# Kernel tuning notes

Hardware: AMD Instinct MI355X
Metric: run time of the kernel (lower is better)

Reference implementation:

```python
import jax, jax.numpy as jnp
import numpy as np

R = 32            # voxel resolution
DIM = 240         # channels C
EPS_NORM = 0.0    # module eps
BN_EPS = 1e-5     # torch BatchNorm1d default eps


def setup_inputs() -> dict:
    key = jax.random.key(0)
    k1, k2, k3 = jax.random.split(key, 3)
    B, C, N = 4, DIM, 32768
    features = jax.random.normal(k1, (B, C, N), jnp.float32)
    coords = jax.random.uniform(k2, (B, 3, N), jnp.float32)
    # mlp params: Conv1d(2C -> C, kernel 1) + BatchNorm1d(C)
    w = jax.random.normal(k3, (C, 2 * C), jnp.float32) / np.sqrt(2 * C).astype(np.float32)
    b = jnp.zeros((C,), jnp.float32)
    gamma = jnp.ones((C,), jnp.float32)
    beta = jnp.zeros((C,), jnp.float32)
    return {"features": features, "coords": coords, "w": w, "b": b, "gamma": gamma, "beta": beta}


def _voxelize(features, coords):
    # normalize coords into [0, 1], scale to voxel grid
    nc = coords - coords.mean(axis=2, keepdims=True)                      # [B,3,N]
    scale = jnp.linalg.norm(nc, axis=1, keepdims=True).max(axis=2, keepdims=True) * 2.0 + EPS_NORM
    nc = nc / scale + 0.5
    nc = jnp.clip(nc * R, 0, R - 1)
    vox = jnp.round(nc).astype(jnp.int32)
    pos = vox[:, 0] + vox[:, 1] * R + vox[:, 2] * (R * R)                 # [B,N] flattened voxel id
    R3 = R * R * R

    def per_batch(f, p):
        # f: [C,N], p: [N] -> [2C, R3]; per-voxel max feature + second (min) feature
        mx = jax.ops.segment_max(f.T, p, num_segments=R3)                 # [R3, C]
        mn = jax.ops.segment_min(f.T, p, num_segments=R3)                 # [R3, C]
        cnt = jax.ops.segment_sum(jnp.ones_like(p), p, num_segments=R3)  # [R3]
        mask = (cnt > 0)[:, None]
        mx = jnp.where(mask, mx, 0.0)
        mn = jnp.where(mask, mn, 0.0)
        return jnp.concatenate([mx, mn], axis=1).T                        # [2C, R3]

    fea = jax.vmap(per_batch)(features, pos)                              # [B,2C,R3]
    return fea, nc


def reference(features, coords, w, b, gamma, beta):
    fea, nc = _voxelize(features, coords)
    # 1x1 Conv1d (pointwise GEMM) + BatchNorm1d (training-mode batch stats) + Swish
    y = jnp.einsum('co,bov->bcv', w, fea) + b[None, :, None]
    mean = y.mean(axis=(0, 2), keepdims=True)
    var = y.var(axis=(0, 2), keepdims=True)
    y = gamma[None, :, None] * (y - mean) * jax.lax.rsqrt(var + BN_EPS) + beta[None, :, None]
    y = y * jax.nn.sigmoid(y)
    B, C, _ = features.shape
    return y.reshape(B, C, R, R, R), nc
```

## Files before the change

kernel.cpp:

```cpp
#include <hip/hip_runtime.h>
#include <cstdint>
#include <cstddef>

#define RR 32
#define R3 32768
#define NPT 32768
#define CH 240
#define CH2 480
#define NB 4
#define Y_ELEMS 31457280

typedef __attribute__((ext_vector_type(8))) short short8v;
typedef __attribute__((ext_vector_type(4))) float float4v;

union u8pack { short8v v; unsigned short u[8]; };

static __device__ __forceinline__ float bf2f(unsigned short u) {
  return __uint_as_float(((unsigned int)u) << 16);
}
static __device__ __forceinline__ unsigned short f2bf(float f) {
  unsigned int u = __float_as_uint(f);
  u = (u + 0x7FFFu + ((u >> 16) & 1u)) >> 16;
  return (unsigned short)u;
}

__global__ void k_init(int* __restrict__ cnt, float* __restrict__ stats,
                       const float* __restrict__ w, unsigned short* __restrict__ wfrag) {
  int g = blockIdx.x * 256 + threadIdx.x;
  if (g < NB * R3) cnt[g] = 0;
  if (g < 4096) stats[g] = 0.0f;
  if (g < 14400) {
    int lane = g & 63, t = g >> 6;
    int mg = t / 75, r = t % 75;
    int kc = r / 5, mL = r % 5;
    int m = mg * 5 + mL;
    int ln = lane & 15, q = lane >> 4;
    const float* src = w + (size_t)(m * 16 + ln) * CH2 + kc * 32 + q * 8;
    u8pack pk;
#pragma unroll
    for (int j = 0; j < 8; j++) pk.u[j] = f2bf(src[j]);
    *(short8v*)&wfrag[(size_t)g * 8] = pk.v;
  }
}

__global__ __launch_bounds__(1024) void k_coord_stats(const float* __restrict__ coords,
                                                      float* __restrict__ ms) {
  __shared__ float red[1024];
  __shared__ float mean[3];
  int b = blockIdx.x, t = threadIdx.x;
  const float4* cb4 = (const float4*)(coords + (size_t)b * 3 * NPT);
  float s[3] = {0.f, 0.f, 0.f};
  for (int i = t; i < NPT / 4; i += 1024) {
#pragma unroll
    for (int d = 0; d < 3; d++) {
      float4 v = cb4[d * (NPT / 4) + i];
      s[d] += (v.x + v.y) + (v.z + v.w);
    }
  }
  for (int d = 0; d < 3; d++) {
    red[t] = s[d]; __syncthreads();
    for (int k = 512; k > 0; k >>= 1) { if (t < k) red[t] += red[t + k]; __syncthreads(); }
    if (t == 0) mean[d] = red[0] * (1.0f / NPT);
    __syncthreads();
  }
  float m0 = mean[0], m1 = mean[1], m2 = mean[2];
  float mx = 0.f;
  for (int i = t; i < NPT / 4; i += 1024) {
    float4 x = cb4[i], y = cb4[NPT / 4 + i], z = cb4[2 * (NPT / 4) + i];
    float dx, dy, dz, n;
    dx = x.x - m0; dy = y.x - m1; dz = z.x - m2; n = dx * dx + dy * dy + dz * dz; mx = fmaxf(mx, n);
    dx = x.y - m0; dy = y.y - m1; dz = z.y - m2; n = dx * dx + dy * dy + dz * dz; mx = fmaxf(mx, n);
    dx = x.z - m0; dy = y.z - m1; dz = z.z - m2; n = dx * dx + dy * dy + dz * dz; mx = fmaxf(mx, n);
    dx = x.w - m0; dy = y.w - m1; dz = z.w - m2; n = dx * dx + dy * dy + dz * dz; mx = fmaxf(mx, n);
  }
  red[t] = mx; __syncthreads();
  for (int k = 512; k > 0; k >>= 1) { if (t < k) red[t] = fmaxf(red[t], red[t + k]); __syncthreads(); }
  if (t == 0) {
    ms[b * 4 + 0] = m0; ms[b * 4 + 1] = m1; ms[b * 4 + 2] = m2;
    ms[b * 4 + 3] = sqrtf(red[0]) * 2.0f;
  }
}

__global__ void k_pos_nc(const float* __restrict__ coords, const float* __restrict__ ms,
                         float* __restrict__ ncout, int* __restrict__ pos, int* __restrict__ cnt) {
  int g = blockIdx.x * 256 + threadIdx.x;
  int b = g >> 15, i = g & (NPT - 1);
  const float* cb = coords + (size_t)b * 3 * NPT;
  float scale = ms[b * 4 + 3];
  int vox[3];
#pragma unroll
  for (int d = 0; d < 3; d++) {
    float v = (cb[(size_t)d * NPT + i] - ms[b * 4 + d]) / scale + 0.5f;
    v = fminf(fmaxf(v * (float)RR, 0.0f), (float)(RR - 1));
    ncout[((size_t)(b * 3 + d)) * NPT + i] = v;
    vox[d] = (int)rintf(v);
  }
  int p = (b << 15) | (vox[0] + (vox[1] << 5) + (vox[2] << 10));
  pos[g] = p;
  atomicAdd(&cnt[p], 1);
}

__global__ void k_scan(const int* __restrict__ cnt, int* __restrict__ offs) {
  __shared__ int part[1024];
  int b = blockIdx.x, t = threadIdx.x;
  const int base = b * R3;
  int local[32];
  int s = 0;
#pragma unroll
  for (int j = 0; j < 32; j++) { local[j] = cnt[base + t * 32 + j]; s += local[j]; }
  part[t] = s; __syncthreads();
  for (int d = 1; d < 1024; d <<= 1) {
    int v = (t >= d) ? part[t - d] : 0;
    __syncthreads();
    part[t] += v;
    __syncthreads();
  }
  int run = (t == 0) ? 0 : part[t - 1];
#pragma unroll
  for (int j = 0; j < 32; j++) { offs[base + t * 32 + j] = run; run += local[j]; }
}

__global__ void k_scatter(const int* __restrict__ pos, int* __restrict__ offs,
                          int* __restrict__ rank) {
  int g = blockIdx.x * 256 + threadIdx.x;
  int p = pos[g];
  int slot = atomicAdd(&offs[p], 1);
  rank[g] = slot;
}

__global__ void k_transpose3(const float* __restrict__ f, const int* __restrict__ rank,
                             unsigned short* __restrict__ fts) {
  __shared__ float tile[CH * 65];
  __shared__ int slts[64];
  int p0 = blockIdx.x * 64, b = blockIdx.y;
  int t = threadIdx.x;
  if (t < 64) slts[t] = rank[b * NPT + p0 + t];
  {
    int pp = t & 63, cq = t >> 6;
    const float* src = f + ((size_t)b * CH) * NPT + p0 + pp;
#pragma unroll 4
    for (int j = 0; j < 60; ++j) {
      int c = j * 4 + cq;
      tile[c * 65 + pp] = src[(size_t)c * NPT];
    }
  }
  __syncthreads();
  int ch8 = t & 7;
#pragma unroll
  for (int pass = 0; pass < 2; ++pass) {
    int p = pass * 32 + (t >> 3);
    unsigned short* dst = fts + ((size_t)(b * NPT + slts[p])) * CH;
#pragma unroll
    for (int i = 0; i < 4; ++i) {
      int ch = ch8 + 8 * i;
      if (ch < 30) {
        u8pack pk;
#pragma unroll
        for (int jj = 0; jj < 8; ++jj) pk.u[jj] = f2bf(tile[(ch * 8 + jj) * 65 + p]);
        *(short8v*)&dst[ch * 8] = pk.v;
      }
    }
  }
}

__global__ __launch_bounds__(512, 4) void k_fused(const int* __restrict__ cnt,
                                                  const int* __restrict__ offs,
                                                  const unsigned short* __restrict__ fts,
                                                  const unsigned short* __restrict__ wfrag,
                                                  const float* __restrict__ bias,
                                                  unsigned short* __restrict__ ybf,
                                                  float* __restrict__ gstats) {
  __shared__ unsigned short fB[4 * 15 * 512];
  __shared__ float bstats[480];
  __shared__ int scnt[64];
  __shared__ int soffs[64];
  int tid = threadIdx.x;
  int wave = tid >> 6, lane = tid & 63;
  int sub = lane >> 5, l = lane & 31;
  int ln = lane & 15, q = lane >> 4;
  int b = blockIdx.y;
  int v0 = blockIdx.x * 64;
  int bbase = b << 15;

  for (int i = tid; i < 480; i += 512) bstats[i] = 0.0f;
  if (tid < 64) scnt[tid] = cnt[bbase + v0 + tid];
  else if (tid < 128) soffs[tid - 64] = offs[bbase + v0 + (tid - 64)];
  __syncthreads();

  int proc = wave * 2 + sub;
  int t1c = 30 + l;
  int kc0 = l >> 2, q0 = l & 3;
  int kc1 = t1c >> 2, q1 = t1c & 3;
#pragma unroll 1
  for (int it = 0; it < 4; ++it) {
    if (l < 30) {
      int lv = it * 16 + proc;
      int ci0 = (q0 * 16 + proc) ^ (kc0 & 7);
      int ci1 = (q1 * 16 + proc) ^ (kc1 & 7);
      int idx0 = ((it * 15 + kc0) * 64 + ci0) * 8;
      int idx1 = ((it * 15 + kc1) * 64 + ci1) * 8;
      int n = scnt[lv];
      if (n == 0) {
        u8pack z;
#pragma unroll
        for (int k = 0; k < 8; k++) z.u[k] = 0;
        *(short8v*)&fB[idx0] = z.v;
        *(short8v*)&fB[idx1] = z.v;
      } else {
        int start = soffs[lv] - n;
        const unsigned short* sp = fts + (size_t)(bbase + start) * CH + l * 8;
        float mx[8], mn[8];
#pragma unroll
        for (int k = 0; k < 8; k++) { mx[k] = -__builtin_inff(); mn[k] = __builtin_inff(); }
        int j = 0;
        for (; j + 8 <= n; j += 8) {
          u8pack u0, u1, u2, u3, u4, u5, u6, u7;
          u0.v = *(const short8v*)(sp);
          u1.v = *(const short8v*)(sp + CH);
          u2.v = *(const short8v*)(sp + 2 * CH);
          u3.v = *(const short8v*)(sp + 3 * CH);
          u4.v = *(const short8v*)(sp + 4 * CH);
          u5.v = *(const short8v*)(sp + 5 * CH);
          u6.v = *(const short8v*)(sp + 6 * CH);
          u7.v = *(const short8v*)(sp + 7 * CH);
          sp += 8 * CH;
#pragma unroll
          for (int k = 0; k < 8; k++) {
            float a0 = bf2f(u0.u[k]), a1 = bf2f(u1.u[k]);
            float a2 = bf2f(u2.u[k]), a3 = bf2f(u3.u[k]);
            float a4 = bf2f(u4.u[k]), a5 = bf2f(u5.u[k]);
            float a6 = bf2f(u6.u[k]), a7 = bf2f(u7.u[k]);
            float hx = fmaxf(fmaxf(fmaxf(a0, a1), fmaxf(a2, a3)),
                             fmaxf(fmaxf(a4, a5), fmaxf(a6, a7)));
            float hn = fminf(fminf(fminf(a0, a1), fminf(a2, a3)),
                             fminf(fminf(a4, a5), fminf(a6, a7)));
            mx[k] = fmaxf(mx[k], hx);
            mn[k] = fminf(mn[k], hn);
          }
        }
        for (; j + 2 <= n; j += 2) {
          u8pack u0, u1;
          u0.v = *(const short8v*)(sp);
          u1.v = *(const short8v*)(sp + CH);
          sp += 2 * CH;
#pragma unroll
          for (int k = 0; k < 8; k++) {
            float a0 = bf2f(u0.u[k]), a1 = bf2f(u1.u[k]);
            mx[k] = fmaxf(mx[k], fmaxf(a0, a1));
            mn[k] = fminf(mn[k], fminf(a0, a1));
          }
        }
        if (j < n) {
          u8pack u0;
          u0.v = *(const short8v*)(sp);
#pragma unroll
          for (int k = 0; k < 8; k++) {
            float a = bf2f(u0.u[k]);
            mx[k] = fmaxf(mx[k], a);
            mn[k] = fminf(mn[k], a);
          }
        }
        u8pack omx, omn;
#pragma unroll
        for (int k = 0; k < 8; k++) { omx.u[k] = f2bf(mx[k]); omn.u[k] = f2bf(mn[k]); }
        *(short8v*)&fB[idx0] = omx.v;
        *(short8v*)&fB[idx1] = omn.v;
      }
    }
  }

  int nmt = (wave == 7) ? 1 : 2;
  short8v wreg[2][15];
#pragma unroll
  for (int mm = 0; mm < 2; ++mm)
    if (mm < nmt) {
      int mt = wave * 2 + mm;
      int mg = mt / 5, mL = mt % 5;
      const unsigned short* wp = wfrag + ((size_t)(mg * 75 + mL) * 512) + lane * 8;
#pragma unroll
      for (int kc = 0; kc < 15; ++kc)
        wreg[mm][kc] = *(const short8v*)(wp + (size_t)kc * 5 * 512);
    }

  __syncthreads();

  float4v acc[2][4];
#pragma unroll
  for (int mm = 0; mm < 2; ++mm)
#pragma unroll
    for (int cg = 0; cg < 4; ++cg) acc[mm][cg] = (float4v){0.f, 0.f, 0.f, 0.f};

#pragma unroll
  for (int kc = 0; kc < 15; ++kc) {
    const unsigned short* fbl = fB + (size_t)((lane ^ (kc & 7)) * 8);
    short8v bf[4];
#pragma unroll
    for (int cg = 0; cg < 4; ++cg)
      bf[cg] = *(const short8v*)(fbl + (size_t)(cg * 15 + kc) * 512);
#pragma unroll
    for (int mm = 0; mm < 2; ++mm)
      if (mm < nmt)
#pragma unroll
        for (int cg = 0; cg < 4; ++cg)
          acc[mm][cg] = __builtin_amdgcn_mfma_f32_16x16x32_bf16(wreg[mm][kc], bf[cg], acc[mm][cg], 0, 0, 0);
  }

  unsigned short* yb = ybf + ((size_t)b * CH) * R3 + v0 + ln;
#pragma unroll
  for (int mm = 0; mm < 2; ++mm)
    if (mm < nmt) {
      int mt = wave * 2 + mm;
#pragma unroll
      for (int r = 0; r < 4; ++r) {
        int c = mt * 16 + q * 4 + r;
        float bb = bias[c];
        unsigned short* yrow = yb + (size_t)c * R3;
        float s = 0.f, sq = 0.f;
#pragma unroll
        for (int cg = 0; cg < 4; ++cg) {
          float yv = acc[mm][cg][r] + bb;
          yrow[cg * 16] = f2bf(yv);
          s += yv; sq += yv * yv;
        }
#pragma unroll
        for (int off = 1; off < 16; off <<= 1) {
          s += __shfl_xor(s, off);
          sq += __shfl_xor(sq, off);
        }
        if (ln == 0) {
          atomicAdd(&bstats[c], s);
          atomicAdd(&bstats[240 + c], sq);
        }
      }
    }
  __syncthreads();
  float* gslot = gstats + (size_t)(blockIdx.x & 7) * 512;
  for (int i = tid; i < 480; i += 512) {
    int g = (i < 240) ? i : (256 + (i - 240));
    atomicAdd(&gslot[g], bstats[(i < 240) ? i : (240 + (i - 240))]);
  }
}

__global__ void k_apply(const unsigned short* __restrict__ ybf, float* __restrict__ out,
                        const float* __restrict__ stats, const float* __restrict__ gamma,
                        const float* __restrict__ beta) {
  int g = blockIdx.x * 256 + threadIdx.x;
  int c = (g >> 12) % CH;
  const float ninv = 1.0f / (float)(NB * R3);
  float sum = 0.f, ssq = 0.f;
#pragma unroll
  for (int sl = 0; sl < 8; ++sl) {
    sum += stats[sl * 512 + c];
    ssq += stats[sl * 512 + 256 + c];
  }
  float mean = sum * ninv;
  float var = ssq * ninv - mean * mean;
  float s = gamma[c] * rsqrtf(var + 1e-5f);
  float h = beta[c] - mean * s;
  u8pack v;
  v.v = *(const short8v*)(ybf + (size_t)g * 8);
  float4 o0, o1;
  float t;
  t = bf2f(v.u[0]) * s + h; o0.x = t / (1.0f + __expf(-t));
  t = bf2f(v.u[1]) * s + h; o0.y = t / (1.0f + __expf(-t));
  t = bf2f(v.u[2]) * s + h; o0.z = t / (1.0f + __expf(-t));
  t = bf2f(v.u[3]) * s + h; o0.w = t / (1.0f + __expf(-t));
  t = bf2f(v.u[4]) * s + h; o1.x = t / (1.0f + __expf(-t));
  t = bf2f(v.u[5]) * s + h; o1.y = t / (1.0f + __expf(-t));
  t = bf2f(v.u[6]) * s + h; o1.z = t / (1.0f + __expf(-t));
  t = bf2f(v.u[7]) * s + h; o1.w = t / (1.0f + __expf(-t));
  ((float4*)out)[(size_t)g * 2] = o0;
  ((float4*)out)[(size_t)g * 2 + 1] = o1;
}

extern "C" void kernel_launch(void* const* d_in, const int* in_sizes, int n_in,
                              void* d_out, int out_size, void* d_ws, size_t ws_size,
                              hipStream_t stream) {
  const float* features = (const float*)d_in[0];
  const float* coords   = (const float*)d_in[1];
  const float* w        = (const float*)d_in[2];
  const float* bias     = (const float*)d_in[3];
  const float* gamma    = (const float*)d_in[4];
  const float* beta     = (const float*)d_in[5];
  float* out = (float*)d_out;

  char* ws = (char*)d_ws;
  size_t off = 0;
  float* ms    = (float*)(ws + off); off += 256;
  float* stats = (float*)(ws + off); off += 16384;
  int* pos     = (int*)(ws + off);   off += (size_t)NB * NPT * 4;
  int* cnt     = (int*)(ws + off);   off += (size_t)NB * R3 * 4;
  int* offs    = (int*)(ws + off);   off += (size_t)NB * R3 * 4;
  int* rank    = (int*)(ws + off);   off += (size_t)NB * NPT * 4;
  unsigned short* wfrag = (unsigned short*)(ws + off); off += (size_t)CH * CH2 * 2;
  unsigned short* fts   = (unsigned short*)(ws + off); off += (size_t)NB * NPT * CH * 2;
  unsigned short* ybf   = (unsigned short*)(ws + off); off += (size_t)NB * R3 * CH * 2;

  float* ncout = out + Y_ELEMS;

  k_init<<<516, 256, 0, stream>>>(cnt, stats, w, wfrag);
  k_coord_stats<<<4, 1024, 0, stream>>>(coords, ms);
  k_pos_nc<<<512, 256, 0, stream>>>(coords, ms, ncout, pos, cnt);
  k_scan<<<4, 1024, 0, stream>>>(cnt, offs);
  k_scatter<<<512, 256, 0, stream>>>(pos, offs, rank);
  k_transpose3<<<dim3(512, 4), 256, 0, stream>>>(features, rank, fts);
  k_fused<<<dim3(512, NB), 512, 0, stream>>>(cnt, offs, fts, wfrag, bias, ybf, stats);
  k_apply<<<Y_ELEMS / 2048, 256, 0, stream>>>(ybf, out, stats, gamma, beta);
}
```

Baseline: 426.8 us.

## Make fused gather-GEMM kernel persistent over four tiles with double-buffered LDS

Each block of the fused voxel max/min gather plus MFMA GEMM kernel now handles four 64-voxel tiles instead of one. The gather for the next tile runs into a second LDS buffer while the current tile's GEMM executes. Weight fragments and bias are loaded once per block, and BN statistics stay in registers, with one global atomic flush at the end instead of per-tile shared-memory atomics. The cost is a doubled LDS footprint, occupancy hint lowered to 2, and only 512 blocks, which may underfill the GPU.

```diff
diff --git a/kernel.cpp b/kernel.cpp
--- a/kernel.cpp
+++ b/kernel.cpp
@@ -163,111 +163,24 @@
   }
 }
 
-__global__ __launch_bounds__(512, 4) void k_fused(const int* __restrict__ cnt,
+__global__ __launch_bounds__(512, 2) void k_fused(const int* __restrict__ cnt,
                                                   const int* __restrict__ offs,
                                                   const unsigned short* __restrict__ fts,
                                                   const unsigned short* __restrict__ wfrag,
                                                   const float* __restrict__ bias,
                                                   unsigned short* __restrict__ ybf,
                                                   float* __restrict__ gstats) {
-  __shared__ unsigned short fB[4 * 15 * 512];
-  __shared__ float bstats[480];
-  __shared__ int scnt[64];
-  __shared__ int soffs[64];
+  __shared__ unsigned short fB[2][4 * 15 * 512];
+  __shared__ int scnt[2][64];
+  __shared__ int soffs[2][64];
+  const int TPB = 4;
   int tid = threadIdx.x;
   int wave = tid >> 6, lane = tid & 63;
   int sub = lane >> 5, l = lane & 31;
   int ln = lane & 15, q = lane >> 4;
-  int b = blockIdx.y;
-  int v0 = blockIdx.x * 64;
+  int T0 = blockIdx.x * TPB;
+  int b = T0 >> 9;
   int bbase = b << 15;
-
-  for (int i = tid; i < 480; i += 512) bstats[i] = 0.0f;
-  if (tid < 64) scnt[tid] = cnt[bbase + v0 + tid];
-  else if (tid < 128) soffs[tid - 64] = offs[bbase + v0 + (tid - 64)];
-  __syncthreads();
-
-  int proc = wave * 2 + sub;
-  int t1c = 30 + l;
-  int kc0 = l >> 2, q0 = l & 3;
-  int kc1 = t1c >> 2, q1 = t1c & 3;
-#pragma unroll 1
-  for (int it = 0; it < 4; ++it) {
-    if (l < 30) {
-      int lv = it * 16 + proc;
-      int ci0 = (q0 * 16 + proc) ^ (kc0 & 7);
-      int ci1 = (q1 * 16 + proc) ^ (kc1 & 7);
-      int idx0 = ((it * 15 + kc0) * 64 + ci0) * 8;
-      int idx1 = ((it * 15 + kc1) * 64 + ci1) * 8;
-      int n = scnt[lv];
-      if (n == 0) {
-        u8pack z;
-#pragma unroll
-        for (int k = 0; k < 8; k++) z.u[k] = 0;
-        *(short8v*)&fB[idx0] = z.v;
-        *(short8v*)&fB[idx1] = z.v;
-      } else {
-        int start = soffs[lv] - n;
-        const unsigned short* sp = fts + (size_t)(bbase + start) * CH + l * 8;
-        float mx[8], mn[8];
-#pragma unroll
-        for (int k = 0; k < 8; k++) { mx[k] = -__builtin_inff(); mn[k] = __builtin_inff(); }
-        int j = 0;
-        for (; j + 8 <= n; j += 8) {
-          u8pack u0, u1, u2, u3, u4, u5, u6, u7;
-          u0.v = *(const short8v*)(sp);
-          u1.v = *(const short8v*)(sp + CH);
-          u2.v = *(const short8v*)(sp + 2 * CH);
-          u3.v = *(const short8v*)(sp + 3 * CH);
-          u4.v = *(const short8v*)(sp + 4 * CH);
-          u5.v = *(const short8v*)(sp + 5 * CH);
-          u6.v = *(const short8v*)(sp + 6 * CH);
-          u7.v = *(const short8v*)(sp + 7 * CH);
-          sp += 8 * CH;
-#pragma unroll
-          for (int k = 0; k < 8; k++) {
-            float a0 = bf2f(u0.u[k]), a1 = bf2f(u1.u[k]);
-            float a2 = bf2f(u2.u[k]), a3 = bf2f(u3.u[k]);
-            float a4 = bf2f(u4.u[k]), a5 = bf2f(u5.u[k]);
-            float a6 = bf2f(u6.u[k]), a7 = bf2f(u7.u[k]);
-            float hx = fmaxf(fmaxf(fmaxf(a0, a1), fmaxf(a2, a3)),
-                             fmaxf(fmaxf(a4, a5), fmaxf(a6, a7)));
-            float hn = fminf(fminf(fminf(a0, a1), fminf(a2, a3)),
-                             fminf(fminf(a4, a5), fminf(a6, a7)));
-            mx[k] = fmaxf(mx[k], hx);
-            mn[k] = fminf(mn[k], hn);
-          }
-        }
-        for (; j + 2 <= n; j += 2) {
-          u8pack u0, u1;
-          u0.v = *(const short8v*)(sp);
-          u1.v = *(const short8v*)(sp + CH);
-          sp += 2 * CH;
-#pragma unroll
-          for (int k = 0; k < 8; k++) {
-            float a0 = bf2f(u0.u[k]), a1 = bf2f(u1.u[k]);
-            mx[k] = fmaxf(mx[k], fmaxf(a0, a1));
-            mn[k] = fminf(mn[k], fminf(a0, a1));
-          }
-        }
-        if (j < n) {
-          u8pack u0;
-          u0.v = *(const short8v*)(sp);
-#pragma unroll
-          for (int k = 0; k < 8; k++) {
-            float a = bf2f(u0.u[k]);
-            mx[k] = fmaxf(mx[k], a);
-            mn[k] = fminf(mn[k], a);
-          }
-        }
-        u8pack omx, omn;
-#pragma unroll
-        for (int k = 0; k < 8; k++) { omx.u[k] = f2bf(mx[k]); omn.u[k] = f2bf(mn[k]); }
-        *(short8v*)&fB[idx0] = omx.v;
-        *(short8v*)&fB[idx1] = omn.v;
-      }
-    }
-  }
 
   int nmt = (wave == 7) ? 1 : 2;
   short8v wreg[2][15];
@@ -282,63 +195,191 @@
         wreg[mm][kc] = *(const short8v*)(wp + (size_t)kc * 5 * 512);
     }
 
-  __syncthreads();
-
-  float4v acc[2][4];
-#pragma unroll
-  for (int mm = 0; mm < 2; ++mm)
-#pragma unroll
-    for (int cg = 0; cg < 4; ++cg) acc[mm][cg] = (float4v){0.f, 0.f, 0.f, 0.f};
-
-#pragma unroll
-  for (int kc = 0; kc < 15; ++kc) {
-    const unsigned short* fbl = fB + (size_t)((lane ^ (kc & 7)) * 8);
-    short8v bf[4];
-#pragma unroll
-    for (int cg = 0; cg < 4; ++cg)
-      bf[cg] = *(const short8v*)(fbl + (size_t)(cg * 15 + kc) * 512);
-#pragma unroll
-    for (int mm = 0; mm < 2; ++mm)
-      if (mm < nmt)
-#pragma unroll
-        for (int cg = 0; cg < 4; ++cg)
-          acc[mm][cg] = __builtin_amdgcn_mfma_f32_16x16x32_bf16(wreg[mm][kc], bf[cg], acc[mm][cg], 0, 0, 0);
-  }
-
-  unsigned short* yb = ybf + ((size_t)b * CH) * R3 + v0 + ln;
+  float bb[2][4];
 #pragma unroll
   for (int mm = 0; mm < 2; ++mm)
     if (mm < nmt) {
       int mt = wave * 2 + mm;
 #pragma unroll
+      for (int r = 0; r < 4; ++r) bb[mm][r] = bias[mt * 16 + q * 4 + r];
+    }
+
+  float sacc[2][4], sqacc[2][4];
+#pragma unroll
+  for (int mm = 0; mm < 2; ++mm)
+#pragma unroll
+    for (int r = 0; r < 4; ++r) { sacc[mm][r] = 0.f; sqacc[mm][r] = 0.f; }
+
+  int proc = wave * 2 + sub;
+  int t1c = 30 + l;
+  int kc0 = l >> 2, q0 = l & 3;
+  int kc1 = t1c >> 2, q1 = t1c & 3;
+  int ci0 = (q0 * 16 + proc) ^ (kc0 & 7);
+  int ci1 = (q1 * 16 + proc) ^ (kc1 & 7);
+
+  auto PRELOAD = [&](int buf, int T) {
+    if (tid < 64) scnt[buf][tid] = cnt[T * 64 + tid];
+    else if (tid < 128) soffs[buf][tid - 64] = offs[T * 64 + (tid - 64)];
+  };
+
+  auto GATHER = [&](int buf, int T) {
+    unsigned short* fb = fB[buf];
+#pragma unroll 1
+    for (int it = 0; it < 4; ++it) {
+      if (l < 30) {
+        int lv = it * 16 + proc;
+        int idx0 = ((it * 15 + kc0) * 64 + ci0) * 8;
+        int idx1 = ((it * 15 + kc1) * 64 + ci1) * 8;
+        int n = scnt[buf][lv];
+        if (n == 0) {
+          u8pack z;
+#pragma unroll
+          for (int k = 0; k < 8; k++) z.u[k] = 0;
+          *(short8v*)&fb[idx0] = z.v;
+          *(short8v*)&fb[idx1] = z.v;
+        } else {
+          int start = soffs[buf][lv] - n;
+          const unsigned short* sp = fts + (size_t)(bbase + start) * CH + l * 8;
+          float mx[8], mn[8];
+#pragma unroll
+          for (int k = 0; k < 8; k++) { mx[k] = -__builtin_inff(); mn[k] = __builtin_inff(); }
+          int j = 0;
+          for (; j + 8 <= n; j += 8) {
+            u8pack u0, u1, u2, u3, u4, u5, u6, u7;
+            u0.v = *(const short8v*)(sp);
+            u1.v = *(const short8v*)(sp + CH);
+            u2.v = *(const short8v*)(sp + 2 * CH);
+            u3.v = *(const short8v*)(sp + 3 * CH);
+            u4.v = *(const short8v*)(sp + 4 * CH);
+            u5.v = *(const short8v*)(sp + 5 * CH);
+            u6.v = *(const short8v*)(sp + 6 * CH);
+            u7.v = *(const short8v*)(sp + 7 * CH);
+            sp += 8 * CH;
+#pragma unroll
+            for (int k = 0; k < 8; k++) {
+              float a0 = bf2f(u0.u[k]), a1 = bf2f(u1.u[k]);
+              float a2 = bf2f(u2.u[k]), a3 = bf2f(u3.u[k]);
+              float a4 = bf2f(u4.u[k]), a5 = bf2f(u5.u[k]);
+              float a6 = bf2f(u6.u[k]), a7 = bf2f(u7.u[k]);
+              float hx = fmaxf(fmaxf(fmaxf(a0, a1), fmaxf(a2, a3)),
+                               fmaxf(fmaxf(a4, a5), fmaxf(a6, a7)));
+              float hn = fminf(fminf(fminf(a0, a1), fminf(a2, a3)),
+                               fminf(fminf(a4, a5), fminf(a6, a7)));
+              mx[k] = fmaxf(mx[k], hx);
+              mn[k] = fminf(mn[k], hn);
+            }
+          }
+          for (; j + 2 <= n; j += 2) {
+            u8pack u0, u1;
+            u0.v = *(const short8v*)(sp);
+            u1.v = *(const short8v*)(sp + CH);
+            sp += 2 * CH;
+#pragma unroll
+            for (int k = 0; k < 8; k++) {
+              float a0 = bf2f(u0.u[k]), a1 = bf2f(u1.u[k]);
+              mx[k] = fmaxf(mx[k], fmaxf(a0, a1));
+              mn[k] = fminf(mn[k], fminf(a0, a1));
+            }
+          }
+          if (j < n) {
+            u8pack u0;
+            u0.v = *(const short8v*)(sp);
+#pragma unroll
+            for (int k = 0; k < 8; k++) {
+              float a = bf2f(u0.u[k]);
+              mx[k] = fmaxf(mx[k], a);
+              mn[k] = fminf(mn[k], a);
+            }
+          }
+          u8pack omx, omn;
+#pragma unroll
+          for (int k = 0; k < 8; k++) { omx.u[k] = f2bf(mx[k]); omn.u[k] = f2bf(mn[k]); }
+          *(short8v*)&fb[idx0] = omx.v;
+          *(short8v*)&fb[idx1] = omn.v;
+        }
+      }
+    }
+  };
+
+  PRELOAD(0, T0);
+  __syncthreads();
+  GATHER(0, T0);
+  PRELOAD(1, T0 + 1);
+  __syncthreads();
+
+#pragma unroll 1
+  for (int i = 0; i < TPB; ++i) {
+    int bufc = i & 1;
+    if (i + 2 < TPB) PRELOAD(bufc, T0 + i + 2);
+    if (i + 1 < TPB) GATHER(bufc ^ 1, T0 + i + 1);
+
+    float4v acc[2][4];
+#pragma unroll
+    for (int mm = 0; mm < 2; ++mm)
+#pragma unroll
+      for (int cg = 0; cg < 4; ++cg) acc[mm][cg] = (float4v){0.f, 0.f, 0.f, 0.f};
+
+    const unsigned short* fbase = fB[bufc];
+#pragma unroll
+    for (int kc = 0; kc < 15; ++kc) {
+      const unsigned short* fbl = fbase + (size_t)((lane ^ (kc & 7)) * 8);
+      short8v bfv[4];
+#pragma unroll
+      for (int cg = 0; cg < 4; ++cg)
+        bfv[cg] = *(const short8v*)(fbl + (size_t)(cg * 15 + kc) * 512);
+#pragma unroll
+      for (int mm = 0; mm < 2; ++mm)
+        if (mm < nmt)
+#pragma unroll
+          for (int cg = 0; cg < 4; ++cg)
+            acc[mm][cg] = __builtin_amdgcn_mfma_f32_16x16x32_bf16(wreg[mm][kc], bfv[cg], acc[mm][cg], 0, 0, 0);
+    }
+
+    int v0 = ((T0 + i) & 511) * 64;
+    unsigned short* yb = ybf + ((size_t)b * CH) * R3 + v0 + ln;
+#pragma unroll
+    for (int mm = 0; mm < 2; ++mm)
+      if (mm < nmt) {
+        int mt = wave * 2 + mm;
+#pragma unroll
+        for (int r = 0; r < 4; ++r) {
+          int c = mt * 16 + q * 4 + r;
+          unsigned short* yrow = yb + (size_t)c * R3;
+          float bbv = bb[mm][r];
+          float s = 0.f, sq = 0.f;
+#pragma unroll
+          for (int cg = 0; cg < 4; ++cg) {
+            float yv = acc[mm][cg][r] + bbv;
+            yrow[cg * 16] = f2bf(yv);
+            s += yv; sq += yv * yv;
+          }
+          sacc[mm][r] += s;
+          sqacc[mm][r] += sq;
+        }
+      }
+    __syncthreads();
+  }
+
+  float* gslot = gstats + (size_t)(blockIdx.x & 7) * 512;
+#pragma unroll
+  for (int mm = 0; mm < 2; ++mm)
+    if (mm < nmt) {
+      int mt = wave * 2 + mm;
+#pragma unroll
       for (int r = 0; r < 4; ++r) {
-        int c = mt * 16 + q * 4 + r;
-        float bb = bias[c];
-        unsigned short* yrow = yb + (size_t)c * R3;
-        float s = 0.f, sq = 0.f;
-#pragma unroll
-        for (int cg = 0; cg < 4; ++cg) {
-          float yv = acc[mm][cg][r] + bb;
-          yrow[cg * 16] = f2bf(yv);
-          s += yv; sq += yv * yv;
-        }
+        float s = sacc[mm][r], sq = sqacc[mm][r];
 #pragma unroll
         for (int off = 1; off < 16; off <<= 1) {
           s += __shfl_xor(s, off);
           sq += __shfl_xor(sq, off);
         }
         if (ln == 0) {
-          atomicAdd(&bstats[c], s);
-          atomicAdd(&bstats[240 + c], sq);
+          int c = mt * 16 + q * 4 + r;
+          atomicAdd(&gslot[c], s);
+          atomicAdd(&gslot[256 + c], sq);
         }
       }
     }
-  __syncthreads();
-  float* gslot = gstats + (size_t)(blockIdx.x & 7) * 512;
-  for (int i = tid; i < 480; i += 512) {
-    int g = (i < 240) ? i : (256 + (i - 240));
-    atomicAdd(&gslot[g], bstats[(i < 240) ? i : (240 + (i - 240))]);
-  }
 }
 
 __global__ void k_apply(const unsigned short* __restrict__ ybf, float* __restrict__ out,
@@ -404,6 +445,6 @@
   k_scan<<<4, 1024, 0, stream>>>(cnt, offs);
   k_scatter<<<512, 256, 0, stream>>>(pos, offs, rank);
   k_transpose3<<<dim3(512, 4), 256, 0, stream>>>(features, rank, fts);
-  k_fused<<<dim3(512, NB), 512, 0, stream>>>(cnt, offs, fts, wfrag, bias, ybf, stats);
+  k_fused<<<512, 512, 0, stream>>>(cnt, offs, fts, wfrag, bias, ybf, stats);
   k_apply<<<Y_ELEMS / 2048, 256, 0, stream>>>(ybf, out, stats, gamma, beta);
 }
```

Measured after the change: 385.7 us. 9.6% less time.

## Make fused voxel-GEMM kernel persistent with dynamic tile and voxel queues

Applied to the files above, without the earlier changes.

Turns k_fused into a persistent kernel of 512 blocks that pull 64-voxel tiles from a global atomic counter. Inside each tile, half-waves take non-empty voxels from an LDS work queue built with a ballot, instead of a fixed voxel-to-wave mapping. BN statistics are kept in registers across tiles and flushed once per block. Weight fragments are streamed with a two-deep register prefetch rather than held as 15 registers. Tail handling is replaced by clamped 8-wide loads. The aim is better load balance across uneven voxel occupancy and less register pressure, at the cost of extra barriers, fB zeroing per tile and reloading weights every tile.

```diff
diff --git a/kernel.cpp b/kernel.cpp
--- a/kernel.cpp
+++ b/kernel.cpp
@@ -8,6 +8,7 @@
 #define CH 240
 #define CH2 480
 #define NB 4
+#define NTILES 2048
 #define Y_ELEMS 31457280
 
 typedef __attribute__((ext_vector_type(8))) short short8v;
@@ -25,8 +26,10 @@
 }
 
 __global__ void k_init(int* __restrict__ cnt, float* __restrict__ stats,
-                       const float* __restrict__ w, unsigned short* __restrict__ wfrag) {
+                       const float* __restrict__ w, unsigned short* __restrict__ wfrag,
+                       int* __restrict__ tilectr) {
   int g = blockIdx.x * 256 + threadIdx.x;
+  if (g == 0) *tilectr = 0;
   if (g < NB * R3) cnt[g] = 0;
   if (g < 4096) stats[g] = 0.0f;
   if (g < 14400) {
@@ -169,61 +172,101 @@
                                                   const unsigned short* __restrict__ wfrag,
                                                   const float* __restrict__ bias,
                                                   unsigned short* __restrict__ ybf,
-                                                  float* __restrict__ gstats) {
+                                                  float* __restrict__ gstats,
+                                                  int* __restrict__ tilectr) {
   __shared__ unsigned short fB[4 * 15 * 512];
-  __shared__ float bstats[480];
-  __shared__ int scnt[64];
-  __shared__ int soffs[64];
+  __shared__ int scnt[64], soffs[64], vlist[64];
+  __shared__ int qh, qm, tilebuf[2];
   int tid = threadIdx.x;
   int wave = tid >> 6, lane = tid & 63;
   int sub = lane >> 5, l = lane & 31;
   int ln = lane & 15, q = lane >> 4;
-  int b = blockIdx.y;
-  int v0 = blockIdx.x * 64;
-  int bbase = b << 15;
-
-  for (int i = tid; i < 480; i += 512) bstats[i] = 0.0f;
-  if (tid < 64) scnt[tid] = cnt[bbase + v0 + tid];
-  else if (tid < 128) soffs[tid - 64] = offs[bbase + v0 + (tid - 64)];
-  __syncthreads();
-
-  int proc = wave * 2 + sub;
+
   int t1c = 30 + l;
   int kc0 = l >> 2, q0 = l & 3;
   int kc1 = t1c >> 2, q1 = t1c & 3;
-#pragma unroll 1
-  for (int it = 0; it < 4; ++it) {
-    if (l < 30) {
-      int lv = it * 16 + proc;
-      int ci0 = (q0 * 16 + proc) ^ (kc0 & 7);
-      int ci1 = (q1 * 16 + proc) ^ (kc1 & 7);
-      int idx0 = ((it * 15 + kc0) * 64 + ci0) * 8;
-      int idx1 = ((it * 15 + kc1) * 64 + ci1) * 8;
+
+  int nmt = (wave == 7) ? 1 : 2;
+  int mt0 = wave * 2, mt1 = wave * 2 + (nmt - 1);
+  const unsigned short* wp0 = wfrag + ((size_t)((mt0 / 5) * 75 + (mt0 % 5)) * 512) + lane * 8;
+  const unsigned short* wp1 = wfrag + ((size_t)((mt1 / 5) * 75 + (mt1 % 5)) * 512) + lane * 8;
+
+  float bb[2][4];
+#pragma unroll
+  for (int mm = 0; mm < 2; ++mm) {
+    int mt = (mm == 0) ? mt0 : mt1;
+#pragma unroll
+    for (int r = 0; r < 4; ++r) bb[mm][r] = bias[mt * 16 + q * 4 + r];
+  }
+  float sacc[2][4], sqacc[2][4];
+#pragma unroll
+  for (int mm = 0; mm < 2; ++mm)
+#pragma unroll
+    for (int r = 0; r < 4; ++r) { sacc[mm][r] = 0.f; sqacc[mm][r] = 0.f; }
+
+  int par = 0;
+  if (tid == 0) tilebuf[0] = atomicAdd(tilectr, 1);
+
+  while (true) {
+    __syncthreads();
+    int T = tilebuf[par];
+    if (T >= NTILES) break;
+    int b = T >> 9;
+    int bbase = b << 15;
+    int v0 = (T & 511) * 64;
+
+    {
+      int4 z4 = {0, 0, 0, 0};
+      for (int i = tid; i < 3840; i += 512) ((int4*)fB)[i] = z4;
+    }
+    if (wave == 0) {
+      int n = cnt[T * 64 + lane];
+      int st = offs[T * 64 + lane];
+      scnt[lane] = n; soffs[lane] = st;
+      unsigned long long mask = __ballot(n > 0);
+      int pfx = __popcll(mask & ((1ull << lane) - 1ull));
+      if (n > 0) vlist[pfx] = lane;
+      if (lane == 0) { qm = __popcll(mask); qh = 0; }
+    }
+    if (tid == 0) tilebuf[par ^ 1] = atomicAdd(tilectr, 1);
+    par ^= 1;
+    __syncthreads();
+
+    int qmL = qm;
+    while (true) {
+      int p;
+      if (l == 0) p = atomicAdd(&qh, 1);
+      p = __shfl(p, sub << 5);
+      if (p >= qmL) break;
+      int lv = vlist[p];
       int n = scnt[lv];
-      if (n == 0) {
-        u8pack z;
-#pragma unroll
-        for (int k = 0; k < 8; k++) z.u[k] = 0;
-        *(short8v*)&fB[idx0] = z.v;
-        *(short8v*)&fB[idx1] = z.v;
-      } else {
-        int start = soffs[lv] - n;
+      int start = soffs[lv] - n;
+      int cg = lv >> 4, cc = lv & 15;
+      if (l < 30) {
         const unsigned short* sp = fts + (size_t)(bbase + start) * CH + l * 8;
+        int lim = (n - 1) * CH;
         float mx[8], mn[8];
 #pragma unroll
         for (int k = 0; k < 8; k++) { mx[k] = -__builtin_inff(); mn[k] = __builtin_inff(); }
-        int j = 0;
-        for (; j + 8 <= n; j += 8) {
+        for (int j = 0; j < n; j += 8) {
+          int base = j * CH;
           u8pack u0, u1, u2, u3, u4, u5, u6, u7;
-          u0.v = *(const short8v*)(sp);
-          u1.v = *(const short8v*)(sp + CH);
-          u2.v = *(const short8v*)(sp + 2 * CH);
-          u3.v = *(const short8v*)(sp + 3 * CH);
-          u4.v = *(const short8v*)(sp + 4 * CH);
-          u5.v = *(const short8v*)(sp + 5 * CH);
-          u6.v = *(const short8v*)(sp + 6 * CH);
-          u7.v = *(const short8v*)(sp + 7 * CH);
-          sp += 8 * CH;
+          int o0 = base;           o0 = o0 < lim ? o0 : lim;
+          int o1 = base + CH;      o1 = o1 < lim ? o1 : lim;
+          int o2 = base + 2 * CH;  o2 = o2 < lim ? o2 : lim;
+          int o3 = base + 3 * CH;  o3 = o3 < lim ? o3 : lim;
+          int o4 = base + 4 * CH;  o4 = o4 < lim ? o4 : lim;
+          int o5 = base + 5 * CH;  o5 = o5 < lim ? o5 : lim;
+          int o6 = base + 6 * CH;  o6 = o6 < lim ? o6 : lim;
+          int o7 = base + 7 * CH;  o7 = o7 < lim ? o7 : lim;
+          u0.v = *(const short8v*)(sp + o0);
+          u1.v = *(const short8v*)(sp + o1);
+          u2.v = *(const short8v*)(sp + o2);
+          u3.v = *(const short8v*)(sp + o3);
+          u4.v = *(const short8v*)(sp + o4);
+          u5.v = *(const short8v*)(sp + o5);
+          u6.v = *(const short8v*)(sp + o6);
+          u7.v = *(const short8v*)(sp + o7);
 #pragma unroll
           for (int k = 0; k < 8; k++) {
             float a0 = bf2f(u0.u[k]), a1 = bf2f(u1.u[k]);
@@ -238,107 +281,93 @@
             mn[k] = fminf(mn[k], hn);
           }
         }
-        for (; j + 2 <= n; j += 2) {
-          u8pack u0, u1;
-          u0.v = *(const short8v*)(sp);
-          u1.v = *(const short8v*)(sp + CH);
-          sp += 2 * CH;
-#pragma unroll
-          for (int k = 0; k < 8; k++) {
-            float a0 = bf2f(u0.u[k]), a1 = bf2f(u1.u[k]);
-            mx[k] = fmaxf(mx[k], fmaxf(a0, a1));
-            mn[k] = fminf(mn[k], fminf(a0, a1));
+        u8pack omx, omn;
+#pragma unroll
+        for (int k = 0; k < 8; k++) { omx.u[k] = f2bf(mx[k]); omn.u[k] = f2bf(mn[k]); }
+        int ci0 = (q0 * 16 + cc) ^ (kc0 & 7);
+        int ci1 = (q1 * 16 + cc) ^ (kc1 & 7);
+        *(short8v*)&fB[((cg * 15 + kc0) * 64 + ci0) * 8] = omx.v;
+        *(short8v*)&fB[((cg * 15 + kc1) * 64 + ci1) * 8] = omn.v;
+      }
+    }
+    __syncthreads();
+
+    float4v acc[2][4];
+#pragma unroll
+    for (int mm = 0; mm < 2; ++mm)
+#pragma unroll
+      for (int cg = 0; cg < 4; ++cg) acc[mm][cg] = (float4v){0.f, 0.f, 0.f, 0.f};
+
+    short8v w0[2], w1[2];
+    w0[0] = *(const short8v*)(wp0);
+    w0[1] = *(const short8v*)(wp0 + 5 * 512);
+    w1[0] = *(const short8v*)(wp1);
+    w1[1] = *(const short8v*)(wp1 + 5 * 512);
+#pragma unroll
+    for (int kc = 0; kc < 15; ++kc) {
+      const unsigned short* fbl = fB + (size_t)((lane ^ (kc & 7)) * 8);
+      short8v bfv[4];
+#pragma unroll
+      for (int cg = 0; cg < 4; ++cg)
+        bfv[cg] = *(const short8v*)(fbl + (size_t)(cg * 15 + kc) * 512);
+      short8v wn0, wn1;
+      if (kc + 2 < 15) {
+        wn0 = *(const short8v*)(wp0 + (size_t)(kc + 2) * 5 * 512);
+        wn1 = *(const short8v*)(wp1 + (size_t)(kc + 2) * 5 * 512);
+      }
+#pragma unroll
+      for (int cg = 0; cg < 4; ++cg)
+        acc[0][cg] = __builtin_amdgcn_mfma_f32_16x16x32_bf16(w0[kc & 1], bfv[cg], acc[0][cg], 0, 0, 0);
+      if (nmt > 1)
+#pragma unroll
+        for (int cg = 0; cg < 4; ++cg)
+          acc[1][cg] = __builtin_amdgcn_mfma_f32_16x16x32_bf16(w1[kc & 1], bfv[cg], acc[1][cg], 0, 0, 0);
+      if (kc + 2 < 15) { w0[kc & 1] = wn0; w1[kc & 1] = wn1; }
+    }
+
+    unsigned short* yb = ybf + ((size_t)b * CH) * R3 + v0 + ln;
+#pragma unroll
+    for (int mm = 0; mm < 2; ++mm)
+      if (mm < nmt) {
+        int mt = (mm == 0) ? mt0 : mt1;
+#pragma unroll
+        for (int r = 0; r < 4; ++r) {
+          int c = mt * 16 + q * 4 + r;
+          unsigned short* yrow = yb + (size_t)c * R3;
+          float bbv = bb[mm][r];
+          float s = 0.f, sq = 0.f;
+#pragma unroll
+          for (int cg = 0; cg < 4; ++cg) {
+            float yv = acc[mm][cg][r] + bbv;
+            yrow[cg * 16] = f2bf(yv);
+            s += yv; sq += yv * yv;
           }
+          sacc[mm][r] += s;
+          sqacc[mm][r] += sq;
         }
-        if (j < n) {
-          u8pack u0;
-          u0.v = *(const short8v*)(sp);
-#pragma unroll
-          for (int k = 0; k < 8; k++) {
-            float a = bf2f(u0.u[k]);
-            mx[k] = fmaxf(mx[k], a);
-            mn[k] = fminf(mn[k], a);
-          }
-        }
-        u8pack omx, omn;
-#pragma unroll
-        for (int k = 0; k < 8; k++) { omx.u[k] = f2bf(mx[k]); omn.u[k] = f2bf(mn[k]); }
-        *(short8v*)&fB[idx0] = omx.v;
-        *(short8v*)&fB[idx1] = omn.v;
       }
-    }
-  }
-
-  int nmt = (wave == 7) ? 1 : 2;
-  short8v wreg[2][15];
+  }
+
+  float* gslot = gstats + (size_t)(blockIdx.x & 7) * 512;
 #pragma unroll
   for (int mm = 0; mm < 2; ++mm)
     if (mm < nmt) {
-      int mt = wave * 2 + mm;
-      int mg = mt / 5, mL = mt % 5;
-      const unsigned short* wp = wfrag + ((size_t)(mg * 75 + mL) * 512) + lane * 8;
-#pragma unroll
-      for (int kc = 0; kc < 15; ++kc)
-        wreg[mm][kc] = *(const short8v*)(wp + (size_t)kc * 5 * 512);
-    }
-
-  __syncthreads();
-
-  float4v acc[2][4];
-#pragma unroll
-  for (int mm = 0; mm < 2; ++mm)
-#pragma unroll
-    for (int cg = 0; cg < 4; ++cg) acc[mm][cg] = (float4v){0.f, 0.f, 0.f, 0.f};
-
-#pragma unroll
-  for (int kc = 0; kc < 15; ++kc) {
-    const unsigned short* fbl = fB + (size_t)((lane ^ (kc & 7)) * 8);
-    short8v bf[4];
-#pragma unroll
-    for (int cg = 0; cg < 4; ++cg)
-      bf[cg] = *(const short8v*)(fbl + (size_t)(cg * 15 + kc) * 512);
-#pragma unroll
-    for (int mm = 0; mm < 2; ++mm)
-      if (mm < nmt)
-#pragma unroll
-        for (int cg = 0; cg < 4; ++cg)
-          acc[mm][cg] = __builtin_amdgcn_mfma_f32_16x16x32_bf16(wreg[mm][kc], bf[cg], acc[mm][cg], 0, 0, 0);
-  }
-
-  unsigned short* yb = ybf + ((size_t)b * CH) * R3 + v0 + ln;
-#pragma unroll
-  for (int mm = 0; mm < 2; ++mm)
-    if (mm < nmt) {
-      int mt = wave * 2 + mm;
+      int mt = (mm == 0) ? mt0 : mt1;
 #pragma unroll
       for (int r = 0; r < 4; ++r) {
-        int c = mt * 16 + q * 4 + r;
-        float bb = bias[c];
-        unsigned short* yrow = yb + (size_t)c * R3;
-        float s = 0.f, sq = 0.f;
-#pragma unroll
-        for (int cg = 0; cg < 4; ++cg) {
-          float yv = acc[mm][cg][r] + bb;
-          yrow[cg * 16] = f2bf(yv);
-          s += yv; sq += yv * yv;
-        }
+        float s = sacc[mm][r], sq = sqacc[mm][r];
 #pragma unroll
         for (int off = 1; off < 16; off <<= 1) {
           s += __shfl_xor(s, off);
           sq += __shfl_xor(sq, off);
         }
         if (ln == 0) {
-          atomicAdd(&bstats[c], s);
-          atomicAdd(&bstats[240 + c], sq);
+          int c = mt * 16 + q * 4 + r;
+          atomicAdd(&gslot[c], s);
+          atomicAdd(&gslot[256 + c], sq);
         }
       }
     }
-  __syncthreads();
-  float* gslot = gstats + (size_t)(blockIdx.x & 7) * 512;
-  for (int i = tid; i < 480; i += 512) {
-    int g = (i < 240) ? i : (256 + (i - 240));
-    atomicAdd(&gslot[g], bstats[(i < 240) ? i : (240 + (i - 240))]);
-  }
 }
 
 __global__ void k_apply(const unsigned short* __restrict__ ybf, float* __restrict__ out,
@@ -387,6 +416,7 @@
   char* ws = (char*)d_ws;
   size_t off = 0;
   float* ms    = (float*)(ws + off); off += 256;
+  int* tilectr = (int*)(ws + off);   off += 256;
   float* stats = (float*)(ws + off); off += 16384;
   int* pos     = (int*)(ws + off);   off += (size_t)NB * NPT * 4;
   int* cnt     = (int*)(ws + off);   off += (size_t)NB * R3 * 4;
@@ -398,12 +428,12 @@
 
   float* ncout = out + Y_ELEMS;
 
-  k_init<<<516, 256, 0, stream>>>(cnt, stats, w, wfrag);
+  k_init<<<516, 256, 0, stream>>>(cnt, stats, w, wfrag, tilectr);
   k_coord_stats<<<4, 1024, 0, stream>>>(coords, ms);
   k_pos_nc<<<512, 256, 0, stream>>>(coords, ms, ncout, pos, cnt);
   k_scan<<<4, 1024, 0, stream>>>(cnt, offs);
   k_scatter<<<512, 256, 0, stream>>>(pos, offs, rank);
   k_transpose3<<<dim3(512, 4), 256, 0, stream>>>(features, rank, fts);
-  k_fused<<<dim3(512, NB), 512, 0, stream>>>(cnt, offs, fts, wfrag, bias, ybf, stats);
+  k_fused<<<512, 512, 0, stream>>>(cnt, offs, fts, wfrag, bias, ybf, stats, tilectr);
   k_apply<<<Y_ELEMS / 2048, 256, 0, stream>>>(ybf, out, stats, gamma, beta);
 }
```

After: 430.1 us. About the same (+0.8%).
